# Performance work log

Hardware: AMD Instinct MI355X
Metric: run time of the kernel (lower is better)

The kernel has to match this reference:

```python
import jax, jax.numpy as jnp
import numpy as np

N, F = 8000, 256
NEG_SLOPE = 0.2


def setup_inputs() -> dict:
    key = jax.random.key(0)
    k1, k2, k3, k4, k5, k6, k7 = jax.random.split(key, 7)
    node_embeddings = jax.random.normal(k1, (N, F), dtype=jnp.float32)
    adj_matrix = jax.random.randint(k2, (N, N), 0, 2, dtype=jnp.int32)
    # Learned params: W (Linear F->F with bias), a (Linear 2F->1 with bias).
    # a's weight [1, 2F] is split into a_src (first F, applied to H_i) and
    # a_dst (last F, applied to H_j) -- mathematically identical to the
    # concat-then-linear formulation, without the N*N*2F intermediate.
    s = 1.0 / np.sqrt(F)
    W_w = jax.random.uniform(k3, (F, F), dtype=jnp.float32, minval=-s, maxval=s)
    W_b = jax.random.uniform(k4, (F,), dtype=jnp.float32, minval=-s, maxval=s)
    s2 = 1.0 / np.sqrt(2 * F)
    a_src = jax.random.uniform(k5, (F,), dtype=jnp.float32, minval=-s2, maxval=s2)
    a_dst = jax.random.uniform(k6, (F,), dtype=jnp.float32, minval=-s2, maxval=s2)
    a_b = jax.random.uniform(k7, (), dtype=jnp.float32, minval=-s2, maxval=s2)
    return {
        "node_embeddings": node_embeddings,
        "adj_matrix": adj_matrix,
        "W_w": W_w,
        "W_b": W_b,
        "a_src": a_src,
        "a_dst": a_dst,
        "a_b": a_b,
    }


def reference(node_embeddings, adj_matrix, W_w, W_b, a_src, a_dst, a_b):
    # H = W(x)
    H = node_embeddings @ W_w.T + W_b                      # [N, F]
    # e_ij = a([H_i ; H_j]) = H_i . a_src + H_j . a_dst + b
    e = (H @ a_src)[:, None] + (H @ a_dst)[None, :] + a_b  # [N, N]
    # mask BEFORE leakyrelu (as in the original), then leakyrelu, then softmax
    e = jnp.where(adj_matrix == 0, -jnp.inf, e)
    e = jnp.where(e >= 0, e, NEG_SLOPE * e)                # leakyrelu(-inf) = -inf
    attn = jax.nn.softmax(e, axis=1)                       # [N, N]
    return attn @ H                                        # [N, F]
```

## Files before the change

kernel.cpp:

```cpp
#include <hip/hip_runtime.h>

#define NN 8000
#define FD 256
#define NEG_SLOPE 0.2f
#define BM 32
#define KT 64
#define NSTEP (NN / KT)

typedef __bf16 bf16;
typedef __bf16 bf16x8 __attribute__((ext_vector_type(8)));
typedef __bf16 bf16x4 __attribute__((ext_vector_type(4)));
typedef float f32x4 __attribute__((ext_vector_type(4)));

__global__ __launch_bounds__(256) void k_linear(const float* __restrict__ X,
                                                const float* __restrict__ W,
                                                const float* __restrict__ b,
                                                bf16* __restrict__ Ht) {
    __shared__ float Xs[16][260];
    const int t = threadIdx.x;
    const int i0 = blockIdx.x * 16;
    #pragma unroll
    for (int r = 0; r < 16; ++r)
        Xs[r][t] = X[(size_t)(i0 + r) * FD + t];
    __syncthreads();
    const int f = t;
    float acc[16];
    const float bf_ = b[f];
    #pragma unroll
    for (int ii = 0; ii < 16; ++ii) acc[ii] = bf_;
    for (int k4 = 0; k4 < FD / 4; ++k4) {
        const float4 w4 = *(const float4*)&W[(size_t)f * FD + k4 * 4];
        #pragma unroll
        for (int ii = 0; ii < 16; ++ii) {
            const float4 x4 = *(const float4*)&Xs[ii][k4 * 4];
            acc[ii] += x4.x * w4.x + x4.y * w4.y + x4.z * w4.z + x4.w * w4.w;
        }
    }
    bf16x8 v0, v1;
    #pragma unroll
    for (int ii = 0; ii < 8; ++ii) { v0[ii] = (bf16)acc[ii]; v1[ii] = (bf16)acc[ii + 8]; }
    *(bf16x8*)&Ht[(size_t)f * NN + i0]     = v0;
    *(bf16x8*)&Ht[(size_t)f * NN + i0 + 8] = v1;
}

__global__ __launch_bounds__(256) void k_attn_vec(const bf16* __restrict__ Ht,
                                                  const float* __restrict__ a_src,
                                                  const float* __restrict__ a_dst,
                                                  const float* __restrict__ a_b,
                                                  float* __restrict__ hs,
                                                  float* __restrict__ hd) {
    __shared__ float psh[4][64], pdh[4][64];
    const int t = threadIdx.x;
    const int li = t & 63;
    const int q = t >> 6;
    const int i = blockIdx.x * 64 + li;
    float ps = 0.f, pd = 0.f;
    #pragma unroll 8
    for (int fi = 0; fi < 64; ++fi) {
        const int f = q * 64 + fi;
        const float h = (float)Ht[(size_t)f * NN + i];
        ps += h * a_src[f];
        pd += h * a_dst[f];
    }
    psh[q][li] = ps; pdh[q][li] = pd;
    __syncthreads();
    if (q == 0) {
        ps = psh[0][li] + psh[1][li] + psh[2][li] + psh[3][li];
        pd = pdh[0][li] + pdh[1][li] + pdh[2][li] + pdh[3][li];
        hs[i] = ps + a_b[0];
        hd[i] = pd;
    }
}

__global__ __launch_bounds__(512) void k_gat(const bf16* __restrict__ Ht,
                                             const int* __restrict__ adj,
                                             const float* __restrict__ hs,
                                             const float* __restrict__ hd,
                                             float* __restrict__ out) {
    __shared__ __attribute__((aligned(16))) bf16 Bt[2][FD * KT];
    __shared__ __attribute__((aligned(16))) bf16 Wt[BM * KT];
    __shared__ float hd_s[NN];
    __shared__ float hs_s[BM];
    __shared__ float l_s[BM];

    const int t  = threadIdx.x;
    const int l  = t & 63;
    const int wv = t >> 6;
    const int i0 = blockIdx.x * BM;

    const int ii = t >> 4;
    const int jm = (t & 15) * 4;
    const int slotW = (t & 15) >> 1;
    const int halfW = (t & 15) & 1;

    const int rs = wv >> 2;
    const int cg = wv & 3;
    const int al = l & 15;
    const int asl = l >> 4;
    const int ar = rs * 16 + al;
    const int arx = ar & 7;
    const int cswz = al & 7;

    {
        float4* hd4 = (float4*)hd_s;
        const float4* hdg = (const float4*)hd;
        for (int k = t; k < NN / 4; k += 512) hd4[k] = hdg[k];
        if (t < BM) hs_s[t] = hs[i0 + t];
    }

    auto stage = [&](int s_, int bufi) {
        const int j0 = s_ * KT;
        #pragma unroll
        for (int q = 0; q < 4; ++q) {
            const int idx16 = t + q * 512;
            const int col = idx16 >> 3;
            const int dslot = idx16 & 7;
            const int sslot = dslot ^ (col & 7);
            const bf16* src = Ht + (size_t)col * NN + j0 + sslot * 8;
            bf16* ldst = &Bt[bufi][(size_t)(wv * 64 + q * 512) * 8];
            __builtin_amdgcn_global_load_lds(
                (const __attribute__((address_space(1))) void*)src,
                (__attribute__((address_space(3))) void*)ldst, 16, 0, 0);
        }
    };

    const size_t adjbase = (size_t)(i0 + ii) * NN + jm;
    int4 adj_cur = *(const int4*)&adj[adjbase];
    stage(0, 0);
    __syncthreads();

    const float hsv = hs_s[ii];
    float lsum = 0.f;
    f32x4 acc0 = {0.f, 0.f, 0.f, 0.f}, acc1 = acc0, acc2 = acc0, acc3 = acc0;

    #pragma unroll 1
    for (int s = 0; s < NSTEP; ++s) {
        const int buf = s & 1;
        int4 adj_nxt;
        if (s < NSTEP - 1) {
            adj_nxt = *(const int4*)&adj[adjbase + (size_t)(s + 1) * KT];
            stage(s + 1, buf ^ 1);
        }
        {
            const float4 hdv = *(const float4*)&hd_s[s * KT + jm];
            bf16x4 wv4;
            float e, w;
            e = hsv + hdv.x; e = e >= 0.f ? e : NEG_SLOPE * e; w = adj_cur.x ? __expf(e) : 0.f; lsum += w; wv4[0] = (bf16)w;
            e = hsv + hdv.y; e = e >= 0.f ? e : NEG_SLOPE * e; w = adj_cur.y ? __expf(e) : 0.f; lsum += w; wv4[1] = (bf16)w;
            e = hsv + hdv.z; e = e >= 0.f ? e : NEG_SLOPE * e; w = adj_cur.z ? __expf(e) : 0.f; lsum += w; wv4[2] = (bf16)w;
            e = hsv + hdv.w; e = e >= 0.f ? e : NEG_SLOPE * e; w = adj_cur.w ? __expf(e) : 0.f; lsum += w; wv4[3] = (bf16)w;
            *(bf16x4*)&Wt[ii * KT + ((slotW ^ (ii & 7)) * 8) + halfW * 4] = wv4;
        }
        if (s < NSTEP - 1) asm volatile("s_waitcnt vmcnt(5) lgkmcnt(0)" ::: "memory");
        else               asm volatile("s_waitcnt vmcnt(0) lgkmcnt(0)" ::: "memory");
        __builtin_amdgcn_s_barrier();
        __builtin_amdgcn_sched_barrier(0);

        {
            const bf16* Wrow = &Wt[ar * KT];
            const bf16x8 a0 = *(const bf16x8*)&Wrow[((0 + asl) ^ arx) * 8];
            const bf16x8 a1 = *(const bf16x8*)&Wrow[((4 + asl) ^ arx) * 8];
            const bf16* Bb = &Bt[buf][0];
            const int colb = cg * 64 + al;
            const bf16x8 b00 = *(const bf16x8*)&Bb[(colb +  0) * KT + ((0 + asl) ^ cswz) * 8];
            const bf16x8 b01 = *(const bf16x8*)&Bb[(colb +  0) * KT + ((4 + asl) ^ cswz) * 8];
            const bf16x8 b10 = *(const bf16x8*)&Bb[(colb + 16) * KT + ((0 + asl) ^ cswz) * 8];
            const bf16x8 b11 = *(const bf16x8*)&Bb[(colb + 16) * KT + ((4 + asl) ^ cswz) * 8];
            const bf16x8 b20 = *(const bf16x8*)&Bb[(colb + 32) * KT + ((0 + asl) ^ cswz) * 8];
            const bf16x8 b21 = *(const bf16x8*)&Bb[(colb + 32) * KT + ((4 + asl) ^ cswz) * 8];
            const bf16x8 b30 = *(const bf16x8*)&Bb[(colb + 48) * KT + ((0 + asl) ^ cswz) * 8];
            const bf16x8 b31 = *(const bf16x8*)&Bb[(colb + 48) * KT + ((4 + asl) ^ cswz) * 8];
            acc0 = __builtin_amdgcn_mfma_f32_16x16x32_bf16(a0, b00, acc0, 0, 0, 0);
            acc0 = __builtin_amdgcn_mfma_f32_16x16x32_bf16(a1, b01, acc0, 0, 0, 0);
            acc1 = __builtin_amdgcn_mfma_f32_16x16x32_bf16(a0, b10, acc1, 0, 0, 0);
            acc1 = __builtin_amdgcn_mfma_f32_16x16x32_bf16(a1, b11, acc1, 0, 0, 0);
            acc2 = __builtin_amdgcn_mfma_f32_16x16x32_bf16(a0, b20, acc2, 0, 0, 0);
            acc2 = __builtin_amdgcn_mfma_f32_16x16x32_bf16(a1, b21, acc2, 0, 0, 0);
            acc3 = __builtin_amdgcn_mfma_f32_16x16x32_bf16(a0, b30, acc3, 0, 0, 0);
            acc3 = __builtin_amdgcn_mfma_f32_16x16x32_bf16(a1, b31, acc3, 0, 0, 0);
        }
        asm volatile("s_waitcnt lgkmcnt(0)" ::: "memory");
        __builtin_amdgcn_s_barrier();
        __builtin_amdgcn_sched_barrier(0);

        adj_cur = adj_nxt;
    }

    lsum += __shfl_xor(lsum, 1);
    lsum += __shfl_xor(lsum, 2);
    lsum += __shfl_xor(lsum, 4);
    lsum += __shfl_xor(lsum, 8);
    if ((l & 15) == 0) l_s[ii] = lsum;
    __syncthreads();

    const int r0 = rs * 16 + asl * 4;
    #pragma unroll
    for (int g = 0; g < 4; ++g) {
        const float rinv = 1.0f / l_s[r0 + g];
        float* orow = out + (size_t)(i0 + r0 + g) * FD + cg * 64 + al;
        orow[0]  = acc0[g] * rinv;
        orow[16] = acc1[g] * rinv;
        orow[32] = acc2[g] * rinv;
        orow[48] = acc3[g] * rinv;
    }
}

extern "C" void kernel_launch(void* const* d_in, const int* in_sizes, int n_in,
                              void* d_out, int out_size, void* d_ws, size_t ws_size,
                              hipStream_t stream) {
    const float* X     = (const float*)d_in[0];
    const int*   adj   = (const int*)d_in[1];
    const float* Ww    = (const float*)d_in[2];
    const float* Wb    = (const float*)d_in[3];
    const float* a_src = (const float*)d_in[4];
    const float* a_dst = (const float*)d_in[5];
    const float* a_b   = (const float*)d_in[6];
    float* out = (float*)d_out;

    bf16*  Ht = (bf16*)d_ws;
    float* hs = (float*)((char*)d_ws + (size_t)FD * NN * sizeof(bf16));
    float* hd = hs + NN;

    k_linear<<<NN / 16, 256, 0, stream>>>(X, Ww, Wb, Ht);
    k_attn_vec<<<NN / 64, 256, 0, stream>>>(Ht, a_src, a_dst, a_b, hs, hd);
    k_gat<<<NN / BM, 512, 0, stream>>>(Ht, adj, hs, hd, out);
}
```

Measured before the change: 181.2 us.

## Split GAT aggregation over key halves with atomic accumulation and direct B loads

The attention-aggregation kernel is split so each row block is handled by two workgroups, each covering half of the neighbor range. Partial outputs and row sums are combined with atomics, and a new normalization kernel divides by the sum. B tiles are loaded straight from global memory into registers instead of being staged in LDS, and the K tile shrinks to 32 with a small double-buffered weight tile. The aim is more parallelism (500 blocks instead of 250) and lower LDS use. The cost is two memsets, an extra kernel launch, atomic traffic, and non-coalesced per-lane global loads of Ht.

Result: slower. 225.3 us (+24.4%).

```diff
diff --git a/kernel.cpp b/kernel.cpp
--- a/kernel.cpp
+++ b/kernel.cpp
@@ -4,12 +4,13 @@
 #define FD 256
 #define NEG_SLOPE 0.2f
 #define BM 32
-#define KT 64
-#define NSTEP (NN / KT)
+#define KT 32
+#define JHALF (NN / 2)
+#define NS (JHALF / KT)
 
 typedef __bf16 bf16;
 typedef __bf16 bf16x8 __attribute__((ext_vector_type(8)));
-typedef __bf16 bf16x4 __attribute__((ext_vector_type(4)));
+typedef __bf16 bf16x2 __attribute__((ext_vector_type(2)));
 typedef float f32x4 __attribute__((ext_vector_type(4)));
 
 __global__ __launch_bounds__(256) void k_linear(const float* __restrict__ X,
@@ -72,137 +73,98 @@
     }
 }
 
-__global__ __launch_bounds__(512) void k_gat(const bf16* __restrict__ Ht,
-                                             const int* __restrict__ adj,
-                                             const float* __restrict__ hs,
-                                             const float* __restrict__ hd,
-                                             float* __restrict__ out) {
-    __shared__ __attribute__((aligned(16))) bf16 Bt[2][FD * KT];
-    __shared__ __attribute__((aligned(16))) bf16 Wt[BM * KT];
-    __shared__ float hd_s[NN];
-    __shared__ float hs_s[BM];
-    __shared__ float l_s[BM];
+__global__ __launch_bounds__(512, 4) void k_gat(const bf16* __restrict__ Ht,
+                                                const int* __restrict__ adj,
+                                                const float* __restrict__ hs,
+                                                const float* __restrict__ hd,
+                                                float* __restrict__ out,
+                                                float* __restrict__ lg) {
+    __shared__ __attribute__((aligned(16))) bf16 Wt[2][4 * 32 * 8];
 
     const int t  = threadIdx.x;
     const int l  = t & 63;
     const int wv = t >> 6;
-    const int i0 = blockIdx.x * BM;
+    const int bid = blockIdx.x;
+    const int ib = bid >> 1, jb = bid & 1;
+    const int i0 = ib * BM;
+    const int j0 = jb * JHALF;
 
-    const int ii = t >> 4;
-    const int jm = (t & 15) * 4;
-    const int slotW = (t & 15) >> 1;
-    const int halfW = (t & 15) & 1;
+    const int row = t >> 4;
+    const int jp  = t & 15;
+    const float hsv = hs[i0 + row];
+    bf16* const wtw[2] = {
+        &Wt[0][(((jp >> 2) * 32) + row) * 8 + (jp & 3) * 2],
+        &Wt[1][(((jp >> 2) * 32) + row) * 8 + (jp & 3) * 2]};
 
-    const int rs = wv >> 2;
-    const int cg = wv & 3;
-    const int al = l & 15;
-    const int asl = l >> 4;
-    const int ar = rs * 16 + al;
-    const int arx = ar & 7;
-    const int cswz = al & 7;
+    const int al = l & 15, asl = l >> 4;
 
-    {
-        float4* hd4 = (float4*)hd_s;
-        const float4* hdg = (const float4*)hd;
-        for (int k = t; k < NN / 4; k += 512) hd4[k] = hdg[k];
-        if (t < BM) hs_s[t] = hs[i0 + t];
-    }
+    const int* adjp = adj + (size_t)(i0 + row) * NN + j0 + jp * 2;
+    const float* hdp = hd + j0 + jp * 2;
+    const bf16* bp0 = Ht + (size_t)(wv * 32 + al) * NN + j0 + asl * 8;
+    const bf16* bp1 = bp0 + (size_t)16 * NN;
 
-    auto stage = [&](int s_, int bufi) {
-        const int j0 = s_ * KT;
-        #pragma unroll
-        for (int q = 0; q < 4; ++q) {
-            const int idx16 = t + q * 512;
-            const int col = idx16 >> 3;
-            const int dslot = idx16 & 7;
-            const int sslot = dslot ^ (col & 7);
-            const bf16* src = Ht + (size_t)col * NN + j0 + sslot * 8;
-            bf16* ldst = &Bt[bufi][(size_t)(wv * 64 + q * 512) * 8];
-            __builtin_amdgcn_global_load_lds(
-                (const __attribute__((address_space(1))) void*)src,
-                (__attribute__((address_space(3))) void*)ldst, 16, 0, 0);
-        }
-    };
+    f32x4 acc00 = {0.f, 0.f, 0.f, 0.f}, acc01 = acc00, acc10 = acc00, acc11 = acc00;
+    float lsum = 0.f;
 
-    const size_t adjbase = (size_t)(i0 + ii) * NN + jm;
-    int4 adj_cur = *(const int4*)&adj[adjbase];
-    stage(0, 0);
-    __syncthreads();
-
-    const float hsv = hs_s[ii];
-    float lsum = 0.f;
-    f32x4 acc0 = {0.f, 0.f, 0.f, 0.f}, acc1 = acc0, acc2 = acc0, acc3 = acc0;
+    int2   adjc = *(const int2*)adjp;
+    float2 hdc  = *(const float2*)hdp;
 
     #pragma unroll 1
-    for (int s = 0; s < NSTEP; ++s) {
-        const int buf = s & 1;
-        int4 adj_nxt;
-        if (s < NSTEP - 1) {
-            adj_nxt = *(const int4*)&adj[adjbase + (size_t)(s + 1) * KT];
-            stage(s + 1, buf ^ 1);
+    for (int s = 0; s < NS; ++s) {
+        const int cur = s & 1;
+        int2 adjn = {0, 0};
+        float2 hdn = {0.f, 0.f};
+        if (s + 1 < NS) {
+            adjn = *(const int2*)(adjp + (size_t)(s + 1) * KT);
+            hdn  = *(const float2*)(hdp + (size_t)(s + 1) * KT);
         }
-        {
-            const float4 hdv = *(const float4*)&hd_s[s * KT + jm];
-            bf16x4 wv4;
-            float e, w;
-            e = hsv + hdv.x; e = e >= 0.f ? e : NEG_SLOPE * e; w = adj_cur.x ? __expf(e) : 0.f; lsum += w; wv4[0] = (bf16)w;
-            e = hsv + hdv.y; e = e >= 0.f ? e : NEG_SLOPE * e; w = adj_cur.y ? __expf(e) : 0.f; lsum += w; wv4[1] = (bf16)w;
-            e = hsv + hdv.z; e = e >= 0.f ? e : NEG_SLOPE * e; w = adj_cur.z ? __expf(e) : 0.f; lsum += w; wv4[2] = (bf16)w;
-            e = hsv + hdv.w; e = e >= 0.f ? e : NEG_SLOPE * e; w = adj_cur.w ? __expf(e) : 0.f; lsum += w; wv4[3] = (bf16)w;
-            *(bf16x4*)&Wt[ii * KT + ((slotW ^ (ii & 7)) * 8) + halfW * 4] = wv4;
-        }
-        if (s < NSTEP - 1) asm volatile("s_waitcnt vmcnt(5) lgkmcnt(0)" ::: "memory");
-        else               asm volatile("s_waitcnt vmcnt(0) lgkmcnt(0)" ::: "memory");
-        __builtin_amdgcn_s_barrier();
-        __builtin_amdgcn_sched_barrier(0);
+        const bf16x8 b0 = *(const bf16x8*)(bp0 + (size_t)s * KT);
+        const bf16x8 b1 = *(const bf16x8*)(bp1 + (size_t)s * KT);
 
-        {
-            const bf16* Wrow = &Wt[ar * KT];
-            const bf16x8 a0 = *(const bf16x8*)&Wrow[((0 + asl) ^ arx) * 8];
-            const bf16x8 a1 = *(const bf16x8*)&Wrow[((4 + asl) ^ arx) * 8];
-            const bf16* Bb = &Bt[buf][0];
-            const int colb = cg * 64 + al;
-            const bf16x8 b00 = *(const bf16x8*)&Bb[(colb +  0) * KT + ((0 + asl) ^ cswz) * 8];
-            const bf16x8 b01 = *(const bf16x8*)&Bb[(colb +  0) * KT + ((4 + asl) ^ cswz) * 8];
-            const bf16x8 b10 = *(const bf16x8*)&Bb[(colb + 16) * KT + ((0 + asl) ^ cswz) * 8];
-            const bf16x8 b11 = *(const bf16x8*)&Bb[(colb + 16) * KT + ((4 + asl) ^ cswz) * 8];
-            const bf16x8 b20 = *(const bf16x8*)&Bb[(colb + 32) * KT + ((0 + asl) ^ cswz) * 8];
-            const bf16x8 b21 = *(const bf16x8*)&Bb[(colb + 32) * KT + ((4 + asl) ^ cswz) * 8];
-            const bf16x8 b30 = *(const bf16x8*)&Bb[(colb + 48) * KT + ((0 + asl) ^ cswz) * 8];
-            const bf16x8 b31 = *(const bf16x8*)&Bb[(colb + 48) * KT + ((4 + asl) ^ cswz) * 8];
-            acc0 = __builtin_amdgcn_mfma_f32_16x16x32_bf16(a0, b00, acc0, 0, 0, 0);
-            acc0 = __builtin_amdgcn_mfma_f32_16x16x32_bf16(a1, b01, acc0, 0, 0, 0);
-            acc1 = __builtin_amdgcn_mfma_f32_16x16x32_bf16(a0, b10, acc1, 0, 0, 0);
-            acc1 = __builtin_amdgcn_mfma_f32_16x16x32_bf16(a1, b11, acc1, 0, 0, 0);
-            acc2 = __builtin_amdgcn_mfma_f32_16x16x32_bf16(a0, b20, acc2, 0, 0, 0);
-            acc2 = __builtin_amdgcn_mfma_f32_16x16x32_bf16(a1, b21, acc2, 0, 0, 0);
-            acc3 = __builtin_amdgcn_mfma_f32_16x16x32_bf16(a0, b30, acc3, 0, 0, 0);
-            acc3 = __builtin_amdgcn_mfma_f32_16x16x32_bf16(a1, b31, acc3, 0, 0, 0);
-        }
+        float e0 = hsv + hdc.x; e0 = e0 >= 0.f ? e0 : NEG_SLOPE * e0;
+        float e1 = hsv + hdc.y; e1 = e1 >= 0.f ? e1 : NEG_SLOPE * e1;
+        const float w0 = adjc.x ? __expf(e0) : 0.f;
+        const float w1 = adjc.y ? __expf(e1) : 0.f;
+        lsum += w0 + w1;
+        bf16x2 wpk; wpk[0] = (bf16)w0; wpk[1] = (bf16)w1;
+        *(bf16x2*)wtw[cur] = wpk;
+
         asm volatile("s_waitcnt lgkmcnt(0)" ::: "memory");
         __builtin_amdgcn_s_barrier();
-        __builtin_amdgcn_sched_barrier(0);
+        asm volatile("" ::: "memory");
 
-        adj_cur = adj_nxt;
+        const bf16* wb = Wt[cur];
+        const bf16x8 a0 = *(const bf16x8*)&wb[(asl * 32 + al) * 8];
+        const bf16x8 a1 = *(const bf16x8*)&wb[(asl * 32 + 16 + al) * 8];
+        acc00 = __builtin_amdgcn_mfma_f32_16x16x32_bf16(a0, b0, acc00, 0, 0, 0);
+        acc01 = __builtin_amdgcn_mfma_f32_16x16x32_bf16(a0, b1, acc01, 0, 0, 0);
+        acc10 = __builtin_amdgcn_mfma_f32_16x16x32_bf16(a1, b0, acc10, 0, 0, 0);
+        acc11 = __builtin_amdgcn_mfma_f32_16x16x32_bf16(a1, b1, acc11, 0, 0, 0);
+
+        adjc = adjn; hdc = hdn;
     }
 
     lsum += __shfl_xor(lsum, 1);
     lsum += __shfl_xor(lsum, 2);
     lsum += __shfl_xor(lsum, 4);
     lsum += __shfl_xor(lsum, 8);
-    if ((l & 15) == 0) l_s[ii] = lsum;
-    __syncthreads();
+    if ((l & 15) == 0) atomicAdd(&lg[i0 + row], lsum);
 
-    const int r0 = rs * 16 + asl * 4;
     #pragma unroll
     for (int g = 0; g < 4; ++g) {
-        const float rinv = 1.0f / l_s[r0 + g];
-        float* orow = out + (size_t)(i0 + r0 + g) * FD + cg * 64 + al;
-        orow[0]  = acc0[g] * rinv;
-        orow[16] = acc1[g] * rinv;
-        orow[32] = acc2[g] * rinv;
-        orow[48] = acc3[g] * rinv;
+        const int r0 = asl * 4 + g;
+        atomicAdd(&out[(size_t)(i0 + r0) * FD + wv * 32 + al],           acc00[g]);
+        atomicAdd(&out[(size_t)(i0 + r0) * FD + wv * 32 + 16 + al],      acc01[g]);
+        atomicAdd(&out[(size_t)(i0 + 16 + r0) * FD + wv * 32 + al],      acc10[g]);
+        atomicAdd(&out[(size_t)(i0 + 16 + r0) * FD + wv * 32 + 16 + al], acc11[g]);
     }
+}
+
+__global__ __launch_bounds__(256) void k_norm(float* __restrict__ out,
+                                              const float* __restrict__ lg) {
+    const int i = blockIdx.x;
+    const float rinv = 1.0f / lg[i];
+    out[(size_t)i * FD + threadIdx.x] *= rinv;
 }
 
 extern "C" void kernel_launch(void* const* d_in, const int* in_sizes, int n_in,
@@ -220,8 +182,13 @@
     bf16*  Ht = (bf16*)d_ws;
     float* hs = (float*)((char*)d_ws + (size_t)FD * NN * sizeof(bf16));
     float* hd = hs + NN;
+    float* lg = hd + NN;
+
+    hipMemsetAsync(out, 0, (size_t)NN * FD * sizeof(float), stream);
+    hipMemsetAsync(lg, 0, NN * sizeof(float), stream);
 
     k_linear<<<NN / 16, 256, 0, stream>>>(X, Ww, Wb, Ht);
     k_attn_vec<<<NN / 64, 256, 0, stream>>>(Ht, a_src, a_dst, a_b, hs, hd);
-    k_gat<<<NN / BM, 512, 0, stream>>>(Ht, adj, hs, hd, out);
+    k_gat<<<(NN / BM) * 2, 512, 0, stream>>>(Ht, adj, hs, hd, out, lg);
+    k_norm<<<NN, 256, 0, stream>>>(out, lg);
 }
```
